# Kernel optimization log

Hardware: AMD Instinct MI355X
Metric: run time of the kernel (lower is better)

Reference implementation:

```python
import jax, jax.numpy as jnp
import numpy as np

B, C_IN, C_OUT, N, K = 4, 128, 128, 4096, 32
BN_EPS = 1e-5


def setup_inputs() -> dict:
    key = jax.random.key(0)
    ks = jax.random.split(key, 12)
    x = jax.random.normal(ks[0], (B, C_IN, N), jnp.float32)
    feature = jax.random.normal(ks[1], (B, C_OUT, N, K), jnp.float32)
    graph_index = jax.random.randint(ks[2], (B, N, K), 0, N)
    s_in = 1.0 / np.sqrt(C_IN)
    s_out = 1.0 / np.sqrt(C_OUT)
    # theta_x: Conv2d(C_IN -> C_IN, 1x1), shared for theta and phi branches
    Wt = jax.random.uniform(ks[3], (C_IN, C_IN), jnp.float32, -s_in, s_in)
    bt = jax.random.uniform(ks[4], (C_IN,), jnp.float32, -s_in, s_in)
    # g: Conv2d(C_OUT -> C_OUT, 1x1)
    Wg = jax.random.uniform(ks[5], (C_OUT, C_OUT), jnp.float32, -s_out, s_out)
    bg = jax.random.uniform(ks[6], (C_OUT,), jnp.float32, -s_out, s_out)
    # W: Conv1d(C_OUT -> C_OUT, 1) followed by BatchNorm1d(C_OUT)
    Ww = jax.random.uniform(ks[7], (C_OUT, C_OUT), jnp.float32, -s_out, s_out)
    bw = jax.random.uniform(ks[8], (C_OUT,), jnp.float32, -s_out, s_out)
    gamma = jnp.ones((C_OUT,), jnp.float32)
    beta = jnp.zeros((C_OUT,), jnp.float32)
    return {"graph_index": graph_index, "x": x, "feature": feature,
            "Wt": Wt, "bt": bt, "Wg": Wg, "bg": bg,
            "Ww": Ww, "bw": bw, "gamma": gamma, "beta": beta}


def reference(graph_index, x, feature, Wt, bt, Wg, bg, Ww, bw, gamma, beta):
    b, c, n = x.shape
    # torch does x.contiguous().view(B, N, C) -> a reshape, not a transpose
    xr = x.reshape(b, n, c)                                   # [B,N,C]
    # index_points: per-batch gather of k neighbors
    batch_idx = jnp.arange(b)[:, None, None]
    nb = xr[batch_idx, graph_index]                           # [B,N,K,C]
    # theta_x 1x1 conv applied to centre and to neighbors (shared weights)
    theta = jnp.einsum('bnc,dc->bnd', xr, Wt) + bt            # [B,N,C]
    phi = jnp.einsum('bnkc,dc->bnkd', nb, Wt) + bt            # [B,N,K,C]
    # local attention logits over k neighbors, softmax over k
    logits = jnp.einsum('bnd,bnkd->bnk', theta, phi)          # [B,N,K]
    coef = jax.nn.softmax(logits, axis=-1)                    # [B,N,K]
    # g 1x1 conv on neighbor value features
    gx = jnp.einsum('bcnk,dc->bnkd', feature, Wg) + bg        # [B,N,K,Cout]
    # weighted aggregation over neighbors
    out = jnp.einsum('bnk,bnkd->bnd', coef, gx)               # [B,N,Cout]
    # W: 1x1 Conv1d then BatchNorm1d (training-mode batch stats)
    y = jnp.einsum('bnd,ed->ben', out, Ww) + bw[None, :, None]  # [B,Cout,N]
    mean = jnp.mean(y, axis=(0, 2), keepdims=True)
    var = jnp.var(y, axis=(0, 2), keepdims=True)
    z = (y - mean) * jax.lax.rsqrt(var + BN_EPS)
    z = z * gamma[None, :, None] + beta[None, :, None]
    return z
```

## Files before the change

kernel.cpp:

```cpp
#include <hip/hip_runtime.h>
#include <hip/hip_bf16.h>

#define BB 4
#define CC 128
#define NN 4096
#define KK 32
#define THETA_OFF  0
#define THETA_SZ   (BB*NN*CC)
#define AGG_OFF    (THETA_OFF + THETA_SZ)
#define AGG_SZ     (BB*NN*CC)
#define M_OFF      (AGG_OFF + AGG_SZ)
#define M_SZ       (CC*CC)
#define B2_OFF     (M_OFF + M_SZ)
#define COEF_OFF   (B2_OFF + 128)
#define COEF_SZ    (BB*NN*KK)
#define PART_OFF   (COEF_OFF + COEF_SZ)
#define PART_SZ    (512*256)
#define PART2_OFF  (PART_OFF + PART_SZ)
#define PART2_SZ   (64*256)

__device__ __forceinline__ float dot4(float4 a, float4 b) {
    return a.x*b.x + a.y*b.y + a.z*b.z + a.w*b.w;
}

__device__ __forceinline__ void async_copy16(const float* g, float* l) {
    __builtin_amdgcn_global_load_lds(
        (const __attribute__((address_space(1))) void*)g,
        (__attribute__((address_space(3))) void*)l, 16, 0, 0);
}

__device__ __forceinline__ int wswz(int e, int q) {
    return (q ^ (e & 7) ^ ((e >> 3) & 3)) * 4;
}

__global__ __launch_bounds__(256) void kWT(const float* __restrict__ x,
                                           const float* __restrict__ Wt,
                                           const float* __restrict__ bt,
                                           float* __restrict__ theta) {
    __shared__ float xr[32][132];
    __shared__ float wt[128][32];
    int t = threadIdx.x;
    long base = (long)blockIdx.x * (32 * 128);
#pragma unroll
    for (int r = 0; r < 4; ++r) {
        int f = (t + 256*r) * 4;
        int dn = f >> 7, c = f & 127;
        *(float4*)&xr[dn][c] = *(const float4*)(x + base + f);
    }
    float acc[4][4] = {};
    int e0 = t & 31, dn0 = (t >> 5) * 4;
    for (int cb = 0; cb < 4; ++cb) {
        __syncthreads();
#pragma unroll
        for (int r = 0; r < 4; ++r) {
            int f = (t + 256*r) * 4;
            int d = f >> 5, cc = f & 31;
            *(float4*)&wt[d][wswz(d, cc >> 2)] = *(const float4*)(Wt + d*128 + cb*32 + cc);
        }
        __syncthreads();
#pragma unroll
        for (int q = 0; q < 8; ++q) {
            int sw = wswz(e0, q);
            float4 a4[4], m4[4];
#pragma unroll
            for (int j = 0; j < 4; ++j) a4[j] = *(const float4*)&xr[dn0+j][cb*32 + q*4];
#pragma unroll
            for (int i = 0; i < 4; ++i) m4[i] = *(const float4*)&wt[e0 + 32*i][sw];
#pragma unroll
            for (int i = 0; i < 4; ++i)
#pragma unroll
                for (int j = 0; j < 4; ++j)
                    acc[i][j] += dot4(a4[j], m4[i]);
        }
    }
    __syncthreads();
#pragma unroll
    for (int i = 0; i < 4; ++i) {
        float b = bt[e0 + 32*i];
#pragma unroll
        for (int j = 0; j < 4; ++j)
            xr[dn0 + j][e0 + 32*i] = acc[i][j] + b;
    }
    __syncthreads();
#pragma unroll
    for (int r = 0; r < 4; ++r) {
        int f = (t + 256*r) * 4;
        int dn = f >> 7, c = f & 127;
        *(float4*)(theta + base + f) = *(const float4*)&xr[dn][c];
    }
}

__global__ __launch_bounds__(256) void kA(const int* __restrict__ gi,
                                          const float* __restrict__ theta,
                                          const float* __restrict__ Ww,
                                          const float* __restrict__ Wg,
                                          const float* __restrict__ bg,
                                          const float* __restrict__ bw,
                                          float* __restrict__ M,
                                          float* __restrict__ b2,
                                          float* __restrict__ coefG) {
    int t = threadIdx.x;
    if (blockIdx.x >= 2048) {
        int bid2 = blockIdx.x - 2048;
        if (bid2 < 64) {
            int e = bid2 * 2 + (t >> 7);
            int c = t & 127;
            float acc = 0.f;
#pragma unroll 8
            for (int d = 0; d < 128; ++d)
                acc += Ww[e*128 + d] * Wg[d*128 + c];
            M[e*128 + c] = acc;
        } else if (t < 128) {
            float acc = bw[t];
            for (int d = 0; d < 128; ++d)
                acc += Ww[t*128 + d] * bg[d];
            b2[t] = acc;
        }
        return;
    }
    __shared__ float tc[8][132];
    __shared__ float logits[8][33];
    int bid = (blockIdx.x & 7) * 256 + (blockIdx.x >> 3);
    long trow0 = (long)bid * 8;
    int b = bid >> 9;
    int k = t >> 3, l8 = t & 7;
    {
        int f = t * 4;
        int dn = f >> 7, c = f & 127;
        *(float4*)&tc[dn][c] = *(const float4*)(theta + trow0*128 + f);
    }
    int idxs[8];
#pragma unroll
    for (int dn = 0; dn < 8; ++dn)
        idxs[dn] = gi[(trow0 + dn) * KK + k];
    __syncthreads();
    const float* tbat = theta + (long)b * NN * CC;
#pragma unroll 2
    for (int dn = 0; dn < 8; ++dn) {
        const float* row = tbat + (long)idxs[dn] * CC;
        float p = 0.f;
#pragma unroll
        for (int j = 0; j < 4; ++j) {
            int c = j*32 + l8*4;
            float4 g = *(const float4*)(row + c);
            float4 tcv = *(const float4*)&tc[dn][c];
            p += dot4(g, tcv);
        }
        p += __shfl_xor(p, 1);
        p += __shfl_xor(p, 2);
        p += __shfl_xor(p, 4);
        if (l8 == 0) logits[dn][k] = p;
    }
    __syncthreads();
    if (t < 64) {
        int row = t >> 3;
        float l[4];
#pragma unroll
        for (int j = 0; j < 4; ++j) l[j] = logits[row][l8 + 8*j];
        float m = fmaxf(fmaxf(l[0], l[1]), fmaxf(l[2], l[3]));
        m = fmaxf(m, __shfl_xor(m, 1));
        m = fmaxf(m, __shfl_xor(m, 2));
        m = fmaxf(m, __shfl_xor(m, 4));
        float e[4]; float s = 0.f;
#pragma unroll
        for (int j = 0; j < 4; ++j) { e[j] = __expf(l[j] - m); s += e[j]; }
        s += __shfl_xor(s, 1);
        s += __shfl_xor(s, 2);
        s += __shfl_xor(s, 4);
        float inv = 1.0f / s;
#pragma unroll
        for (int j = 0; j < 4; ++j)
            coefG[(trow0 + row) * KK + l8 + 8*j] = e[j] * inv;
    }
}

__global__ __launch_bounds__(256) void kB(const float* __restrict__ coefG,
                                          const float* __restrict__ feat,
                                          float* __restrict__ aggG) {
    __shared__ float stage[4][2][1024];
    __shared__ float aggL[32][36];
    int t = threadIdx.x;
    int cc4 = blockIdx.x & 3;
    int tile = blockIdx.x >> 2;
    int b = tile >> 7;
    int n0 = (tile & 127) * 32;
    int w = t >> 6, lane = t & 63;
    int r8 = lane >> 3, ks = lane & 7;

    float4 cf[4];
#pragma unroll
    for (int j = 0; j < 4; ++j)
        cf[j] = *(const float4*)(coefG + ((size_t)tile * 32 + j*8 + r8) * KK + ks * 4);
#pragma unroll
    for (int j = 0; j < 4; ++j)
        asm volatile("" :: "v"(cf[j].x), "v"(cf[j].y), "v"(cf[j].z), "v"(cf[j].w));

    const size_t S = (size_t)NN * KK;
    const float* fbase = feat + ((size_t)b * CC + cc4 * 32) * S + (size_t)n0 * KK + lane * 4;
    float* myStage = &stage[w][0][0];

#pragma unroll
    for (int ch = 0; ch < 2; ++ch) {
        const float* fc = fbase + (size_t)(ch * 4 + w) * S;
        float* ld = myStage + ch * 1024;
#pragma unroll
        for (int i = 0; i < 4; ++i)
            async_copy16(fc + i * 256, ld + i * 256);
    }

#pragma unroll
    for (int ch = 0; ch < 8; ++ch) {
        if (ch < 7) asm volatile("s_waitcnt vmcnt(4)" ::: "memory");
        else        asm volatile("s_waitcnt vmcnt(0)" ::: "memory");
        const float* sl = myStage + (ch & 1) * 1024 + lane * 4;
        float v[4];
#pragma unroll
        for (int j = 0; j < 4; ++j) {
            float4 f = *(const float4*)(sl + j * 256);
            v[j] = dot4(f, cf[j]);
        }
#pragma unroll
        for (int j = 0; j < 4; ++j) {
            v[j] += __shfl_xor(v[j], 1);
            v[j] += __shfl_xor(v[j], 2);
            v[j] += __shfl_xor(v[j], 4);
        }
        if (ks == 0) {
#pragma unroll
            for (int j = 0; j < 4; ++j)
                aggL[j*8 + r8][ch * 4 + w] = v[j];
        }
        if (ch + 2 < 8) {
            const float* fc = fbase + (size_t)((ch + 2) * 4 + w) * S;
            float* ld = myStage + (ch & 1) * 1024;
#pragma unroll
            for (int i = 0; i < 4; ++i)
                async_copy16(fc + i * 256, ld + i * 256);
        }
    }
    __syncthreads();
    int orow = t >> 3, col4 = (t & 7) * 4;
    *(float4*)(aggG + ((size_t)b * NN + n0 + orow) * CC + cc4 * 32 + col4) =
        *(const float4*)&aggL[orow][col4];
}

__global__ __launch_bounds__(256) void kC(const float* __restrict__ aggG,
                                          const float* __restrict__ Mmat,
                                          const float* __restrict__ b2v,
                                          float* __restrict__ y,
                                          float* __restrict__ partial) {
    __shared__ float agg[32][132];
    __shared__ float mc[128][32];
    __shared__ float pw[4][128];
    __shared__ float qw[4][128];
    int t = threadIdx.x;
    int b = blockIdx.x >> 7;
    int n0 = (blockIdx.x & 127) * 32;
    long base = (long)blockIdx.x * (32 * 128);
#pragma unroll
    for (int r = 0; r < 4; ++r) {
        int f = (t + 256*r) * 4;
        int dn = f >> 7, c = f & 127;
        *(float4*)&agg[dn][c] = *(const float4*)(aggG + base + f);
    }
    float acc[4][4] = {};
    int e0 = t & 31, dn0 = (t >> 5) * 4;
    for (int cb = 0; cb < 4; ++cb) {
        __syncthreads();
#pragma unroll
        for (int r = 0; r < 4; ++r) {
            int f = (t + 256*r) * 4;
            int e = f >> 5, cc = f & 31;
            *(float4*)&mc[e][wswz(e, cc >> 2)] = *(const float4*)(Mmat + e*128 + cb*32 + cc);
        }
        __syncthreads();
#pragma unroll
        for (int q = 0; q < 8; ++q) {
            int sw = wswz(e0, q);
            float4 a4[4], m4[4];
#pragma unroll
            for (int j = 0; j < 4; ++j) a4[j] = *(const float4*)&agg[dn0+j][cb*32 + q*4];
#pragma unroll
            for (int i = 0; i < 4; ++i) m4[i] = *(const float4*)&mc[e0 + 32*i][sw];
#pragma unroll
            for (int i = 0; i < 4; ++i)
#pragma unroll
                for (int j = 0; j < 4; ++j)
                    acc[i][j] += dot4(a4[j], m4[i]);
        }
        __syncthreads();
    }
    int w = t >> 6;
#pragma unroll
    for (int i = 0; i < 4; ++i) {
        int e = e0 + 32*i;
        float bb = b2v[e];
        float4 yv;
        yv.x = acc[i][0] + bb;
        yv.y = acc[i][1] + bb;
        yv.z = acc[i][2] + bb;
        yv.w = acc[i][3] + bb;
        *(float4*)(y + ((long)(b*CC + e)) * NN + n0 + dn0) = yv;
        float s = yv.x + yv.y + yv.z + yv.w;
        float qq = yv.x*yv.x + yv.y*yv.y + yv.z*yv.z + yv.w*yv.w;
        s  += __shfl_xor(s, 32);
        qq += __shfl_xor(qq, 32);
        if (!(t & 32)) { pw[w][e] = s; qw[w][e] = qq; }
    }
    __syncthreads();
    if (t < 128) {
        partial[(long)blockIdx.x * 256 + t]       = pw[0][t] + pw[1][t] + pw[2][t] + pw[3][t];
        partial[(long)blockIdx.x * 256 + 128 + t] = qw[0][t] + qw[1][t] + qw[2][t] + qw[3][t];
    }
}

__global__ __launch_bounds__(256) void kR1(const float* __restrict__ partial,
                                           float* __restrict__ partial2) {
    int t = threadIdx.x;
    long b0 = (long)blockIdx.x * 8;
    float acc = 0.f;
#pragma unroll
    for (int j = 0; j < 8; ++j)
        acc += partial[(b0 + j) * 256 + t];
    partial2[(long)blockIdx.x * 256 + t] = acc;
}

__global__ __launch_bounds__(256) void kZf(float* __restrict__ y,
                                           const float* __restrict__ partial2,
                                           const float* __restrict__ gamma,
                                           const float* __restrict__ beta) {
    __shared__ float buf[256];
    __shared__ float scs[128];
    __shared__ float shs[128];
    int t = threadIdx.x;
    float acc = 0.f;
#pragma unroll 8
    for (int j = 0; j < 64; ++j)
        acc += partial2[j * 256 + t];
    buf[t] = acc;
    __syncthreads();
    if (t < 128) {
        float S = buf[t], Q = buf[t + 128];
        const float invN = 1.0f / (BB * NN);
        float mean = S * invN;
        float var  = Q * invN - mean * mean;
        float sc = rsqrtf(var + 1e-5f) * gamma[t];
        scs[t] = sc;
        shs[t] = beta[t] - mean * sc;
    }
    __syncthreads();
    int idx = blockIdx.x * 256 + t;
#pragma unroll
    for (int r = 0; r < 2; ++r) {
        int i = idx + r * 262144;
        int e = (i >> 10) & 127;
        float sc = scs[e], sh = shs[e];
        float4 v = ((float4*)y)[i];
        v.x = v.x * sc + sh;
        v.y = v.y * sc + sh;
        v.z = v.z * sc + sh;
        v.w = v.w * sc + sh;
        ((float4*)y)[i] = v;
    }
}

extern "C" void kernel_launch(void* const* d_in, const int* in_sizes, int n_in,
                              void* d_out, int out_size, void* d_ws, size_t ws_size,
                              hipStream_t stream) {
    const int*   gi    = (const int*)d_in[0];
    const float* x     = (const float*)d_in[1];
    const float* feat  = (const float*)d_in[2];
    const float* Wt    = (const float*)d_in[3];
    const float* bt    = (const float*)d_in[4];
    const float* Wg    = (const float*)d_in[5];
    const float* bg    = (const float*)d_in[6];
    const float* Ww    = (const float*)d_in[7];
    const float* bw    = (const float*)d_in[8];
    const float* gamma = (const float*)d_in[9];
    const float* beta  = (const float*)d_in[10];

    float* y  = (float*)d_out;
    float* ws = (float*)d_ws;
    float* theta    = ws + THETA_OFF;
    float* aggG     = ws + AGG_OFF;
    float* Mmat     = ws + M_OFF;
    float* b2       = ws + B2_OFF;
    float* coefG    = ws + COEF_OFF;
    float* partial  = ws + PART_OFF;
    float* partial2 = ws + PART2_OFF;

    kWT<<<512, 256, 0, stream>>>(x, Wt, bt, theta);
    kA<<<2113, 256, 0, stream>>>(gi, theta, Ww, Wg, bg, bw, Mmat, b2, coefG);
    kB<<<2048, 256, 0, stream>>>(coefG, feat, aggG);
    kC<<<512, 256, 0, stream>>>(aggG, Mmat, b2, y, partial);
    kR1<<<64, 256, 0, stream>>>(partial, partial2);
    kZf<<<1024, 256, 0, stream>>>(y, partial2, gamma, beta);
}
```

Baseline: 102.1 us.

## Fuse neighbor aggregation and output projection into one kernel

```diff
diff --git a/kernel.cpp b/kernel.cpp
--- a/kernel.cpp
+++ b/kernel.cpp
@@ -7,15 +7,13 @@
 #define KK 32
 #define THETA_OFF  0
 #define THETA_SZ   (BB*NN*CC)
-#define AGG_OFF    (THETA_OFF + THETA_SZ)
-#define AGG_SZ     (BB*NN*CC)
-#define M_OFF      (AGG_OFF + AGG_SZ)
+#define M_OFF      (THETA_OFF + THETA_SZ)
 #define M_SZ       (CC*CC)
 #define B2_OFF     (M_OFF + M_SZ)
 #define COEF_OFF   (B2_OFF + 128)
 #define COEF_SZ    (BB*NN*KK)
 #define PART_OFF   (COEF_OFF + COEF_SZ)
-#define PART_SZ    (512*256)
+#define PART_SZ    (1024*256)
 #define PART2_OFF  (PART_OFF + PART_SZ)
 #define PART2_SZ   (64*256)
 
@@ -174,97 +172,66 @@
     }
 }
 
-__global__ __launch_bounds__(256) void kB(const float* __restrict__ coefG,
-                                          const float* __restrict__ feat,
-                                          float* __restrict__ aggG) {
-    __shared__ float stage[4][2][1024];
-    __shared__ float aggL[32][36];
-    int t = threadIdx.x;
-    int cc4 = blockIdx.x & 3;
-    int tile = blockIdx.x >> 2;
-    int b = tile >> 7;
-    int n0 = (tile & 127) * 32;
+__global__ __launch_bounds__(256) void kBC(const float* __restrict__ coefG,
+                                           const float* __restrict__ feat,
+                                           const float* __restrict__ Mmat,
+                                           const float* __restrict__ b2v,
+                                           float* __restrict__ y,
+                                           float* __restrict__ partial) {
+    __shared__ float ring[4][2][512];
+    __shared__ float aggL[16][132];
+    int t = threadIdx.x;
+    int bid = (blockIdx.x & 7) * 128 + (blockIdx.x >> 3);
+    int b = bid >> 8;
+    int n0 = (bid & 255) * 16;
+    long trow0 = (long)bid * 16;
     int w = t >> 6, lane = t & 63;
     int r8 = lane >> 3, ks = lane & 7;
 
-    float4 cf[4];
-#pragma unroll
-    for (int j = 0; j < 4; ++j)
-        cf[j] = *(const float4*)(coefG + ((size_t)tile * 32 + j*8 + r8) * KK + ks * 4);
-#pragma unroll
-    for (int j = 0; j < 4; ++j)
-        asm volatile("" :: "v"(cf[j].x), "v"(cf[j].y), "v"(cf[j].z), "v"(cf[j].w));
+    float4 cf0 = *(const float4*)(coefG + (trow0 + r8) * KK + ks * 4);
+    float4 cf1 = *(const float4*)(coefG + (trow0 + 8 + r8) * KK + ks * 4);
+    asm volatile("" :: "v"(cf0.x), "v"(cf0.y), "v"(cf0.z), "v"(cf0.w));
+    asm volatile("" :: "v"(cf1.x), "v"(cf1.y), "v"(cf1.z), "v"(cf1.w));
 
     const size_t S = (size_t)NN * KK;
-    const float* fbase = feat + ((size_t)b * CC + cc4 * 32) * S + (size_t)n0 * KK + lane * 4;
-    float* myStage = &stage[w][0][0];
+    const float* fbase = feat + (size_t)b * CC * S + (size_t)n0 * KK + lane * 4;
+    float* myRing = &ring[w][0][0];
 
 #pragma unroll
     for (int ch = 0; ch < 2; ++ch) {
         const float* fc = fbase + (size_t)(ch * 4 + w) * S;
-        float* ld = myStage + ch * 1024;
-#pragma unroll
-        for (int i = 0; i < 4; ++i)
-            async_copy16(fc + i * 256, ld + i * 256);
-    }
-
-#pragma unroll
-    for (int ch = 0; ch < 8; ++ch) {
-        if (ch < 7) asm volatile("s_waitcnt vmcnt(4)" ::: "memory");
-        else        asm volatile("s_waitcnt vmcnt(0)" ::: "memory");
-        const float* sl = myStage + (ch & 1) * 1024 + lane * 4;
-        float v[4];
-#pragma unroll
-        for (int j = 0; j < 4; ++j) {
-            float4 f = *(const float4*)(sl + j * 256);
-            v[j] = dot4(f, cf[j]);
-        }
-#pragma unroll
-        for (int j = 0; j < 4; ++j) {
-            v[j] += __shfl_xor(v[j], 1);
-            v[j] += __shfl_xor(v[j], 2);
-            v[j] += __shfl_xor(v[j], 4);
-        }
+        float* ld = myRing + ch * 512;
+        async_copy16(fc, ld);
+        async_copy16(fc + 256, ld + 256);
+    }
+
+#pragma unroll
+    for (int ch = 0; ch < 32; ++ch) {
+        if (ch < 31) asm volatile("s_waitcnt vmcnt(2)" ::: "memory");
+        else         asm volatile("s_waitcnt vmcnt(0)" ::: "memory");
+        const float* sl = myRing + (ch & 1) * 512 + lane * 4;
+        float4 f0 = *(const float4*)(sl);
+        float4 f1 = *(const float4*)(sl + 256);
+        float v0 = dot4(f0, cf0);
+        float v1 = dot4(f1, cf1);
+        v0 += __shfl_xor(v0, 1); v0 += __shfl_xor(v0, 2); v0 += __shfl_xor(v0, 4);
+        v1 += __shfl_xor(v1, 1); v1 += __shfl_xor(v1, 2); v1 += __shfl_xor(v1, 4);
         if (ks == 0) {
-#pragma unroll
-            for (int j = 0; j < 4; ++j)
-                aggL[j*8 + r8][ch * 4 + w] = v[j];
-        }
-        if (ch + 2 < 8) {
+            aggL[r8][ch * 4 + w]     = v0;
+            aggL[8 + r8][ch * 4 + w] = v1;
+        }
+        if (ch + 2 < 32) {
             const float* fc = fbase + (size_t)((ch + 2) * 4 + w) * S;
-            float* ld = myStage + (ch & 1) * 1024;
-#pragma unroll
-            for (int i = 0; i < 4; ++i)
-                async_copy16(fc + i * 256, ld + i * 256);
-        }
-    }
-    __syncthreads();
-    int orow = t >> 3, col4 = (t & 7) * 4;
-    *(float4*)(aggG + ((size_t)b * NN + n0 + orow) * CC + cc4 * 32 + col4) =
-        *(const float4*)&aggL[orow][col4];
-}
-
-__global__ __launch_bounds__(256) void kC(const float* __restrict__ aggG,
-                                          const float* __restrict__ Mmat,
-                                          const float* __restrict__ b2v,
-                                          float* __restrict__ y,
-                                          float* __restrict__ partial) {
-    __shared__ float agg[32][132];
-    __shared__ float mc[128][32];
-    __shared__ float pw[4][128];
-    __shared__ float qw[4][128];
-    int t = threadIdx.x;
-    int b = blockIdx.x >> 7;
-    int n0 = (blockIdx.x & 127) * 32;
-    long base = (long)blockIdx.x * (32 * 128);
-#pragma unroll
-    for (int r = 0; r < 4; ++r) {
-        int f = (t + 256*r) * 4;
-        int dn = f >> 7, c = f & 127;
-        *(float4*)&agg[dn][c] = *(const float4*)(aggG + base + f);
-    }
-    float acc[4][4] = {};
-    int e0 = t & 31, dn0 = (t >> 5) * 4;
+            float* ld = myRing + (ch & 1) * 512;
+            async_copy16(fc, ld);
+            async_copy16(fc + 256, ld + 256);
+        }
+    }
+    __syncthreads();
+
+    float (*mc)[32] = (float(*)[32])&ring[0][0][0];
+    float acc[4][2] = {};
+    int e0 = t & 31, dn0 = (t >> 5) * 2;
     for (int cb = 0; cb < 4; ++cb) {
         __syncthreads();
 #pragma unroll
@@ -277,50 +244,56 @@
 #pragma unroll
         for (int q = 0; q < 8; ++q) {
             int sw = wswz(e0, q);
-            float4 a4[4], m4[4];
-#pragma unroll
-            for (int j = 0; j < 4; ++j) a4[j] = *(const float4*)&agg[dn0+j][cb*32 + q*4];
+            float4 a4[2], m4[4];
+#pragma unroll
+            for (int j = 0; j < 2; ++j) a4[j] = *(const float4*)&aggL[dn0+j][cb*32 + q*4];
 #pragma unroll
             for (int i = 0; i < 4; ++i) m4[i] = *(const float4*)&mc[e0 + 32*i][sw];
 #pragma unroll
             for (int i = 0; i < 4; ++i)
 #pragma unroll
-                for (int j = 0; j < 4; ++j)
+                for (int j = 0; j < 2; ++j)
                     acc[i][j] += dot4(a4[j], m4[i]);
         }
-        __syncthreads();
-    }
-    int w = t >> 6;
+    }
+    __syncthreads();
+    float (*yT)[20] = (float(*)[20])&ring[0][0][0];
 #pragma unroll
     for (int i = 0; i < 4; ++i) {
         int e = e0 + 32*i;
         float bb = b2v[e];
-        float4 yv;
-        yv.x = acc[i][0] + bb;
-        yv.y = acc[i][1] + bb;
-        yv.z = acc[i][2] + bb;
-        yv.w = acc[i][3] + bb;
-        *(float4*)(y + ((long)(b*CC + e)) * NN + n0 + dn0) = yv;
-        float s = yv.x + yv.y + yv.z + yv.w;
-        float qq = yv.x*yv.x + yv.y*yv.y + yv.z*yv.z + yv.w*yv.w;
-        s  += __shfl_xor(s, 32);
-        qq += __shfl_xor(qq, 32);
-        if (!(t & 32)) { pw[w][e] = s; qw[w][e] = qq; }
-    }
-    __syncthreads();
+#pragma unroll
+        for (int j = 0; j < 2; ++j)
+            yT[e][dn0 + j] = acc[i][j] + bb;
+    }
+    __syncthreads();
+    {
+        int e = t >> 1, half = t & 1;
+        float4 v0 = *(const float4*)&yT[e][half * 8];
+        float4 v1 = *(const float4*)&yT[e][half * 8 + 4];
+        float* dst = y + ((size_t)(b*CC + e)) * NN + n0 + half * 8;
+        *(float4*)dst       = v0;
+        *(float4*)(dst + 4) = v1;
+    }
     if (t < 128) {
-        partial[(long)blockIdx.x * 256 + t]       = pw[0][t] + pw[1][t] + pw[2][t] + pw[3][t];
-        partial[(long)blockIdx.x * 256 + 128 + t] = qw[0][t] + qw[1][t] + qw[2][t] + qw[3][t];
+        float s = 0.f, q = 0.f;
+#pragma unroll
+        for (int j = 0; j < 16; ++j) {
+            float v = yT[t][j];
+            s += v; q += v * v;
+        }
+        partial[(size_t)bid * 256 + t]       = s;
+        partial[(size_t)bid * 256 + 128 + t] = q;
     }
 }
 
 __global__ __launch_bounds__(256) void kR1(const float* __restrict__ partial,
                                            float* __restrict__ partial2) {
     int t = threadIdx.x;
-    long b0 = (long)blockIdx.x * 8;
+    long b0 = (long)blockIdx.x * 16;
     float acc = 0.f;
 #pragma unroll
-    for (int j = 0; j < 8; ++j)
+    for (int j = 0; j < 16; ++j)
         acc += partial[(b0 + j) * 256 + t];
     partial2[(long)blockIdx.x * 256 + t] = acc;
 }
@@ -382,7 +355,6 @@
     float* y  = (float*)d_out;
     float* ws = (float*)d_ws;
     float* theta    = ws + THETA_OFF;
-    float* aggG     = ws + AGG_OFF;
     float* Mmat     = ws + M_OFF;
     float* b2       = ws + B2_OFF;
     float* coefG    = ws + COEF_OFF;
@@ -391,8 +363,7 @@
 
     kWT<<<512, 256, 0, stream>>>(x, Wt, bt, theta);
     kA<<<2113, 256, 0, stream>>>(gi, theta, Ww, Wg, bg, bw, Mmat, b2, coefG);
-    kB<<<2048, 256, 0, stream>>>(coefG, feat, aggG);
-    kC<<<512, 256, 0, stream>>>(aggG, Mmat, b2, y, partial);
+    kBC<<<1024, 256, 0, stream>>>(coefG, feat, Mmat, b2, y, partial);
     kR1<<<64, 256, 0, stream>>>(partial, partial2);
     kZf<<<1024, 256, 0, stream>>>(y, partial2, gamma, beta);
 }
```

Result: faster. 94.97 us (median of 2 runs) (-7.0%).
